# Performance work log

Hardware: AMD Instinct MI355X
Metric: run time of the kernel (lower is better)

The kernel has to match this reference:

```python
import jax, jax.numpy as jnp
import numpy as np

B, H, S, D = 2, 8, 4096, 64

def setup_inputs() -> dict:
    key = jax.random.key(0)
    kq, kk, kv = jax.random.split(key, 3)
    queries = jax.random.normal(kq, (B, H, S, D), dtype=jnp.float32)
    keys = jax.random.normal(kk, (B, H, S, D), dtype=jnp.float32)
    values = jax.random.normal(kv, (B, H, S, D), dtype=jnp.float32)
    adj = jnp.zeros((1,), dtype=jnp.int32)  # unused by the module, kept for signature fidelity
    return {"queries": queries, "keys": keys, "values": values, "adj": adj}

def reference(queries, keys, values, adj):
    # scores: [B,H,S,S]; note the original divides by a hard-coded 16, not sqrt(d)
    scores = jnp.einsum('bhqd,bhkd->bhqk', queries, keys) / 16.0
    attn = jax.nn.softmax(scores, axis=-1)
    # dropout p=0.0 -> identity in eval/deterministic mode
    h = jnp.einsum('bhqk,bhkd->bhqd', attn, values)  # [B,H,S,D]
    # original uses .view (a reshape, NOT a transpose) to (S, B, H, D)
    return jnp.reshape(h, (S, B, H, D))
```

## Files before the change

kernel.cpp:

```cpp
#include <hip/hip_runtime.h>
#include <hip/hip_bf16.h>
#include <math.h>

#define S_LEN 4096
#define D_DIM 64
#define NBH   16
#define HKT   32
#define QPRE  0.09016844f

typedef __attribute__((ext_vector_type(8))) short bf16x8;
typedef __attribute__((ext_vector_type(4))) float f32x4;
typedef __attribute__((ext_vector_type(4))) __fp16 f16x4;
typedef __attribute__((ext_vector_type(2))) __fp16 f16x2;

__device__ __forceinline__ unsigned int pkbf(float lo, float hi) {
  unsigned int ua = __float_as_uint(lo) + 0x8000u;
  unsigned int ub = __float_as_uint(hi) + 0x8000u;
  return __builtin_amdgcn_perm(ub, ua, 0x07060302u);
}
__device__ __forceinline__ unsigned int pkhf(float lo, float hi) {
  f16x2 h = __builtin_amdgcn_cvt_pkrtz(lo, hi);
  return *(unsigned int*)&h;
}
__device__ __forceinline__ void dma16(const unsigned short* g, unsigned short* l) {
  __builtin_amdgcn_global_load_lds(
      (const __attribute__((address_space(1))) unsigned int*)g,
      (__attribute__((address_space(3))) unsigned int*)l, 16, 0, 0);
}

__global__ __launch_bounds__(256) void prep(const float* __restrict__ K,
                                            const float* __restrict__ V,
                                            unsigned short* __restrict__ Kbf,
                                            unsigned short* __restrict__ Vt) {
  const int tid = threadIdx.x;
  __shared__ unsigned short tile[64][72];
  if (blockIdx.x < 256) {
    const int bh = blockIdx.x >> 4, ch = blockIdx.x & 15;
    const size_t base = ((size_t)bh * S_LEN + ch * 256) * D_DIM;
#pragma unroll
    for (int p = 0; p < 8; ++p) {
      int i = tid + p * 256;
      int row = i >> 3, c = (i & 7) * 8;
      float4 a = *(const float4*)&K[base + row * D_DIM + c];
      float4 b = *(const float4*)&K[base + row * D_DIM + c + 4];
      uint4 w;
      w.x = pkbf(a.x, a.y); w.y = pkbf(a.z, a.w);
      w.z = pkbf(b.x, b.y); w.w = pkbf(b.z, b.w);
      *(uint4*)&Kbf[base + row * D_DIM + c] = w;
    }
    return;
  }
  const int blk = blockIdx.x - 256;
  const int bh = blk >> 6, kt = blk & 63;
  const float* src = V + ((size_t)bh * S_LEN + kt * 64) * D_DIM;
#pragma unroll
  for (int p = 0; p < 4; ++p) {
    int i = tid + p * 256;
    int row = i >> 4, c = (i & 15) * 4;
    float4 f = *(const float4*)&src[row * D_DIM + c];
    int cs = c ^ (((row >> 4) & 3) << 4);
    unsigned long long w = (unsigned long long)pkhf(f.x, f.y) |
                           ((unsigned long long)pkhf(f.z, f.w) << 32);
    *(unsigned long long*)&tile[row][cs] = w;
  }
  __syncthreads();
  const int kc = tid & 7;
#pragma unroll
  for (int p = 0; p < 2; ++p) {
    int d = p * 32 + (tid >> 3);
    int col = d ^ (((kc >> 1) & 3) << 4);
    union { unsigned short u[8]; uint4 v; } t;
#pragma unroll
    for (int i = 0; i < 8; ++i) t.u[i] = tile[kc * 8 + i][col];
    *(uint4*)&Vt[((size_t)bh * D_DIM + d) * S_LEN + kt * 64 + kc * 8] = t.v;
  }
}

__global__ __launch_bounds__(256, 4) void fattn(const float* __restrict__ Q,
                                                const unsigned short* __restrict__ Kbf,
                                                const unsigned short* __restrict__ Vt,
                                                unsigned short* __restrict__ Oh,
                                                float* __restrict__ Lw) {
  const int bh   = blockIdx.x & 15;
  const int qb   = (blockIdx.x >> 4) & 31;
  const int half = blockIdx.x >> 9;
  const int tid  = threadIdx.x;
  const int wave = tid >> 6;
  const int lane = tid & 63;
  const int quad = lane >> 4;
  const int l15  = lane & 15;
  const int rho  = l15 & 7;
  const int T0   = half * HKT;

  __shared__ unsigned short Ksh[2][64][64];
  __shared__ unsigned short Vsh[2][64][64];

  bf16x8 qf[2][2];
#pragma unroll
  for (int qt = 0; qt < 2; ++qt) {
    const int qg = qb * 128 + wave * 32 + qt * 16 + l15;
    const float* qp = Q + ((size_t)bh * S_LEN + qg) * D_DIM + quad * 8;
#pragma unroll
    for (int h = 0; h < 2; ++h) {
      float4 a = *(const float4*)&qp[h * 32];
      float4 b = *(const float4*)&qp[h * 32 + 4];
      union { unsigned int u[4]; bf16x8 v; } f;
      f.u[0] = pkbf(a.x * QPRE, a.y * QPRE);
      f.u[1] = pkbf(a.z * QPRE, a.w * QPRE);
      f.u[2] = pkbf(b.x * QPRE, b.y * QPRE);
      f.u[3] = pkbf(b.z * QPRE, b.w * QPRE);
      qf[qt][h] = f.v;
    }
  }

  f32x4 ot[2][4];
#pragma unroll
  for (int qt = 0; qt < 2; ++qt)
#pragma unroll
    for (int dt = 0; dt < 4; ++dt) ot[qt][dt] = (f32x4){0.f, 0.f, 0.f, 0.f};
  float Lp[2] = {0.f, 0.f};

  const unsigned short* Kb = Kbf + (size_t)bh * S_LEN * D_DIM;
  const unsigned short* Vb = Vt + (size_t)bh * D_DIM * S_LEN;

  const int r_lo = wave * 8 + (lane >> 3);
  const int csrc = ((lane & 7) ^ (lane >> 3)) * 8;

  const int ck0 = (quad ^ rho) * 8;
  const int ck1 = ((quad + 4) ^ rho) * 8;
  const int vrow  = l15 * 128 + (quad & 1) * 8;
  const int rho16 = rho << 4;
  const int vq2   = (quad >> 1) << 4;

#define DMAK(T, B) do { const int t_ = (T); \
  dma16(&Kb[(size_t)(t_ * 64 + r_lo) * 64 + csrc],      &Ksh[B][wave * 8][0]); \
  dma16(&Kb[(size_t)(t_ * 64 + r_lo + 32) * 64 + csrc], &Ksh[B][wave * 8 + 32][0]); } while (0)
#define DMAV(T, B) do { const int t_ = (T); \
  dma16(&Vb[(size_t)r_lo * S_LEN + t_ * 64 + csrc],        &Vsh[B][wave * 8][0]); \
  dma16(&Vb[(size_t)(r_lo + 32) * S_LEN + t_ * 64 + csrc], &Vsh[B][wave * 8 + 32][0]); } while (0)

#define SCORES(KB, PD) do { \
  _Pragma("unroll") \
  for (int mt = 0; mt < 4; ++mt) { \
    const int row_ = mt * 16 + l15; \
    bf16x8 kf0 = *(const bf16x8*)&Ksh[KB][row_][ck0]; \
    bf16x8 kf1 = *(const bf16x8*)&Ksh[KB][row_][ck1]; \
    _Pragma("unroll") \
    for (int qt = 0; qt < 2; ++qt) { \
      f32x4 acc = (f32x4){0.f, 0.f, 0.f, 0.f}; \
      acc = __builtin_amdgcn_mfma_f32_16x16x32_bf16(kf0, qf[qt][0], acc, 0, 0, 0); \
      acc = __builtin_amdgcn_mfma_f32_16x16x32_bf16(kf1, qf[qt][1], acc, 0, 0, 0); \
      float p0 = __builtin_amdgcn_exp2f(acc[0]); \
      float p1 = __builtin_amdgcn_exp2f(acc[1]); \
      float p2 = __builtin_amdgcn_exp2f(acc[2]); \
      float p3 = __builtin_amdgcn_exp2f(acc[3]); \
      Lp[qt] += (p0 + p1) + (p2 + p3); \
      PD[mt][qt][0] = pkhf(p0, p1); \
      PD[mt][qt][1] = pkhf(p2, p3); \
    } \
  } } while (0)

#define PVSTEP(VB, PU) do { \
  const char* vbase = (const char*)&Vsh[VB][0][0]; \
  _Pragma("unroll") \
  for (int mt = 0; mt < 4; ++mt) { \
    const int vb_ = vrow + (((mt << 5) + vq2) ^ rho16); \
    union { unsigned int u[2]; f16x4 v; } pb0, pb1; \
    pb0.u[0] = PU[mt][0][0]; pb0.u[1] = PU[mt][0][1]; \
    pb1.u[0] = PU[mt][1][0]; pb1.u[1] = PU[mt][1][1]; \
    _Pragma("unroll") \
    for (int dt = 0; dt < 4; ++dt) { \
      f16x4 va = *(const f16x4*)(vbase + vb_ + dt * 2048); \
      ot[0][dt] = __builtin_amdgcn_mfma_f32_16x16x16f16(va, pb0.v, ot[0][dt], 0, 0, 0); \
      ot[1][dt] = __builtin_amdgcn_mfma_f32_16x16x16f16(va, pb1.v, ot[1][dt], 0, 0, 0); \
    } \
  } } while (0)

#define ITER(I, KBL, KBU, VBL, VBU, PU, PD) do { \
  __syncthreads(); \
  if ((I) < HKT - 2) DMAK(T0 + (I) + 2, KBL); \
  DMAV(T0 + (I) + 1, VBL); \
  SCORES(KBU, PD); \
  PVSTEP(VBU, PU); } while (0)

  unsigned int pA[4][2][2], pB[4][2][2];

  DMAK(T0, 0); DMAV(T0, 0);
  __syncthreads();
  SCORES(0, pA);
  DMAK(T0 + 1, 1);

  for (int b = 0; b < HKT - 2; b += 2) {
    ITER(b + 0, 0, 1, 1, 0, pA, pB);
    ITER(b + 1, 1, 0, 0, 1, pB, pA);
  }
  ITER(HKT - 2, 0, 1, 1, 0, pA, pB);
  __syncthreads();
  PVSTEP(1, pB);

#pragma unroll
  for (int qt = 0; qt < 2; ++qt) {
    float Lt = Lp[qt];
    Lt += __shfl_xor(Lt, 16);
    Lt += __shfl_xor(Lt, 32);
    const size_t grow = (size_t)bh * S_LEN + qb * 128 + wave * 32 + qt * 16 + l15;
    if (quad == 0) Lw[grow * 2 + half] = Lt;
#pragma unroll
    for (int dt = 0; dt < 4; ++dt) {
      uint2 w;
      w.x = pkhf(ot[qt][dt][0], ot[qt][dt][1]);
      w.y = pkhf(ot[qt][dt][2], ot[qt][dt][3]);
      *(uint2*)&Oh[grow * 128 + half * 64 + dt * 16 + quad * 4] = w;
    }
  }
#undef DMAK
#undef DMAV
#undef SCORES
#undef PVSTEP
#undef ITER
}

__global__ __launch_bounds__(256) void reduce(unsigned short* Oh, const float* __restrict__ Lw) {
  const int tid = threadIdx.x;
  const size_t r = (size_t)blockIdx.x * 32 + (tid >> 3);
  const int d0 = (tid & 7) * 8;
  union { uint4 v; __fp16 h[8]; } a, b;
  a.v = *(const uint4*)&Oh[r * 128 + d0];
  b.v = *(const uint4*)&Oh[r * 128 + 64 + d0];
  const float linv = 1.0f / (Lw[r * 2] + Lw[r * 2 + 1]);
  float o[8];
#pragma unroll
  for (int j = 0; j < 8; ++j) o[j] = ((float)a.h[j] + (float)b.h[j]) * linv;
  __syncthreads();
  float* Of = (float*)Oh;
  float4 w0 = {o[0], o[1], o[2], o[3]};
  float4 w1 = {o[4], o[5], o[6], o[7]};
  *(float4*)&Of[r * 64 + d0]     = w0;
  *(float4*)&Of[r * 64 + d0 + 4] = w1;
}

extern "C" void kernel_launch(void* const* d_in, const int* in_sizes, int n_in,
                              void* d_out, int out_size, void* d_ws, size_t ws_size,
                              hipStream_t stream) {
  const float* Q = (const float*)d_in[0];
  const float* K = (const float*)d_in[1];
  const float* V = (const float*)d_in[2];
  unsigned short* Kbf = (unsigned short*)d_ws;
  unsigned short* Vt  = Kbf + (size_t)NBH * S_LEN * D_DIM;
  float* Lw = (float*)(Vt + (size_t)NBH * S_LEN * D_DIM);
  unsigned short* Oh = (unsigned short*)d_out;

  prep<<<1280, 256, 0, stream>>>(K, V, Kbf, Vt);
  fattn<<<NBH * 32 * 2, 256, 0, stream>>>(Q, Kbf, Vt, Oh, Lw);
  reduce<<<(NBH * S_LEN) / 32, 256, 0, stream>>>(Oh, Lw);
}
```

Before: 184.3 us.

## Switch attention MFMAs to 32x32x16 tiles with permlane32 swap for P layout

```diff
diff --git a/kernel.cpp b/kernel.cpp
--- a/kernel.cpp
+++ b/kernel.cpp
@@ -10,8 +10,10 @@
 
 typedef __attribute__((ext_vector_type(8))) short bf16x8;
 typedef __attribute__((ext_vector_type(4))) float f32x4;
-typedef __attribute__((ext_vector_type(4))) __fp16 f16x4;
+typedef __attribute__((ext_vector_type(16))) float f32x16;
+typedef __attribute__((ext_vector_type(8))) __fp16 f16x8;
 typedef __attribute__((ext_vector_type(2))) __fp16 f16x2;
+typedef __attribute__((ext_vector_type(2))) unsigned int u32x2;
 
 __device__ __forceinline__ unsigned int pkbf(float lo, float hi) {
   unsigned int ua = __float_as_uint(lo) + 0x8000u;
@@ -87,50 +89,38 @@
   const int tid  = threadIdx.x;
   const int wave = tid >> 6;
   const int lane = tid & 63;
-  const int quad = lane >> 4;
-  const int l15  = lane & 15;
-  const int rho  = l15 & 7;
+  const int l31  = lane & 31;
+  const int hi   = lane >> 5;
   const int T0   = half * HKT;
 
   __shared__ unsigned short Ksh[2][64][64];
   __shared__ unsigned short Vsh[2][64][64];
 
-  bf16x8 qf[2][2];
-#pragma unroll
-  for (int qt = 0; qt < 2; ++qt) {
-    const int qg = qb * 128 + wave * 32 + qt * 16 + l15;
-    const float* qp = Q + ((size_t)bh * S_LEN + qg) * D_DIM + quad * 8;
-#pragma unroll
-    for (int h = 0; h < 2; ++h) {
-      float4 a = *(const float4*)&qp[h * 32];
-      float4 b = *(const float4*)&qp[h * 32 + 4];
+  bf16x8 qf2[4];
+  {
+    const int qg = qb * 128 + wave * 32 + l31;
+    const float* qp = Q + ((size_t)bh * S_LEN + qg) * D_DIM + hi * 8;
+#pragma unroll
+    for (int dm = 0; dm < 4; ++dm) {
+      float4 a = *(const float4*)&qp[dm * 16];
+      float4 b = *(const float4*)&qp[dm * 16 + 4];
       union { unsigned int u[4]; bf16x8 v; } f;
       f.u[0] = pkbf(a.x * QPRE, a.y * QPRE);
       f.u[1] = pkbf(a.z * QPRE, a.w * QPRE);
       f.u[2] = pkbf(b.x * QPRE, b.y * QPRE);
       f.u[3] = pkbf(b.z * QPRE, b.w * QPRE);
-      qf[qt][h] = f.v;
+      qf2[dm] = f.v;
     }
   }
 
-  f32x4 ot[2][4];
-#pragma unroll
-  for (int qt = 0; qt < 2; ++qt)
-#pragma unroll
-    for (int dt = 0; dt < 4; ++dt) ot[qt][dt] = (f32x4){0.f, 0.f, 0.f, 0.f};
-  float Lp[2] = {0.f, 0.f};
+  f32x16 ov[2] = {{}, {}};
+  float Lt = 0.f;
 
   const unsigned short* Kb = Kbf + (size_t)bh * S_LEN * D_DIM;
   const unsigned short* Vb = Vt + (size_t)bh * D_DIM * S_LEN;
 
   const int r_lo = wave * 8 + (lane >> 3);
   const int csrc = ((lane & 7) ^ (lane >> 3)) * 8;
-
-  const int ck0 = (quad ^ rho) * 8;
-  const int ck1 = ((quad + 4) ^ rho) * 8;
-  const int vrow  = l15 * 128 + (quad & 1) * 8;
-  const int rho16 = rho << 4;
-  const int vq2   = (quad >> 1) << 4;
 
 #define DMAK(T, B) do { const int t_ = (T); \
   dma16(&Kb[(size_t)(t_ * 64 + r_lo) * 64 + csrc],      &Ksh[B][wave * 8][0]); \
@@ -140,39 +130,47 @@
   dma16(&Vb[(size_t)(r_lo + 32) * S_LEN + t_ * 64 + csrc], &Vsh[B][wave * 8 + 32][0]); } while (0)
 
 #define SCORES(KB, PD) do { \
+  const char* kbase_ = (const char*)&Ksh[KB][0][0]; \
   _Pragma("unroll") \
-  for (int mt = 0; mt < 4; ++mt) { \
-    const int row_ = mt * 16 + l15; \
-    bf16x8 kf0 = *(const bf16x8*)&Ksh[KB][row_][ck0]; \
-    bf16x8 kf1 = *(const bf16x8*)&Ksh[KB][row_][ck1]; \
+  for (int kt2 = 0; kt2 < 2; ++kt2) { \
+    const int krow_ = kt2 * 32 + l31; \
+    f32x16 acc2 = {}; \
     _Pragma("unroll") \
-    for (int qt = 0; qt < 2; ++qt) { \
-      f32x4 acc = (f32x4){0.f, 0.f, 0.f, 0.f}; \
-      acc = __builtin_amdgcn_mfma_f32_16x16x32_bf16(kf0, qf[qt][0], acc, 0, 0, 0); \
-      acc = __builtin_amdgcn_mfma_f32_16x16x32_bf16(kf1, qf[qt][1], acc, 0, 0, 0); \
-      float p0 = __builtin_amdgcn_exp2f(acc[0]); \
-      float p1 = __builtin_amdgcn_exp2f(acc[1]); \
-      float p2 = __builtin_amdgcn_exp2f(acc[2]); \
-      float p3 = __builtin_amdgcn_exp2f(acc[3]); \
-      Lp[qt] += (p0 + p1) + (p2 + p3); \
-      PD[mt][qt][0] = pkhf(p0, p1); \
-      PD[mt][qt][1] = pkhf(p2, p3); \
+    for (int dm = 0; dm < 4; ++dm) { \
+      bf16x8 kf = *(const bf16x8*)(kbase_ + krow_ * 128 + (((dm * 2 + hi) ^ (krow_ & 7)) * 16)); \
+      acc2 = __builtin_amdgcn_mfma_f32_32x32x16_bf16(kf, qf2[dm], acc2, 0, 0, 0); \
     } \
+    float pp[16]; \
+    _Pragma("unroll") \
+    for (int j = 0; j < 16; ++j) pp[j] = __builtin_amdgcn_exp2f(acc2[j]); \
+    Lt += (((pp[0] + pp[1]) + (pp[2] + pp[3])) + ((pp[4] + pp[5]) + (pp[6] + pp[7]))) \
+        + (((pp[8] + pp[9]) + (pp[10] + pp[11])) + ((pp[12] + pp[13]) + (pp[14] + pp[15]))); \
+    unsigned int w00 = pkhf(pp[0], pp[1]),   w01 = pkhf(pp[2], pp[3]); \
+    unsigned int w10 = pkhf(pp[4], pp[5]),   w11 = pkhf(pp[6], pp[7]); \
+    unsigned int w20 = pkhf(pp[8], pp[9]),   w21 = pkhf(pp[10], pp[11]); \
+    unsigned int w30 = pkhf(pp[12], pp[13]), w31 = pkhf(pp[14], pp[15]); \
+    u32x2 s0 = __builtin_amdgcn_permlane32_swap(w00, w10, false, false); \
+    u32x2 s1 = __builtin_amdgcn_permlane32_swap(w01, w11, false, false); \
+    u32x2 s2 = __builtin_amdgcn_permlane32_swap(w20, w30, false, false); \
+    u32x2 s3 = __builtin_amdgcn_permlane32_swap(w21, w31, false, false); \
+    PD[kt2 * 2 + 0][0] = s0.x; PD[kt2 * 2 + 0][1] = s1.x; \
+    PD[kt2 * 2 + 0][2] = s0.y; PD[kt2 * 2 + 0][3] = s1.y; \
+    PD[kt2 * 2 + 1][0] = s2.x; PD[kt2 * 2 + 1][1] = s3.x; \
+    PD[kt2 * 2 + 1][2] = s2.y; PD[kt2 * 2 + 1][3] = s3.y; \
   } } while (0)
 
 #define PVSTEP(VB, PU) do { \
-  const char* vbase = (const char*)&Vsh[VB][0][0]; \
+  const char* vbase_ = (const char*)&Vsh[VB][0][0]; \
   _Pragma("unroll") \
-  for (int mt = 0; mt < 4; ++mt) { \
-    const int vb_ = vrow + (((mt << 5) + vq2) ^ rho16); \
-    union { unsigned int u[2]; f16x4 v; } pb0, pb1; \
-    pb0.u[0] = PU[mt][0][0]; pb0.u[1] = PU[mt][0][1]; \
-    pb1.u[0] = PU[mt][1][0]; pb1.u[1] = PU[mt][1][1]; \
+  for (int dt2 = 0; dt2 < 2; ++dt2) { \
+    const int drow_ = dt2 * 32 + l31; \
     _Pragma("unroll") \
-    for (int dt = 0; dt < 4; ++dt) { \
-      f16x4 va = *(const f16x4*)(vbase + vb_ + dt * 2048); \
-      ot[0][dt] = __builtin_amdgcn_mfma_f32_16x16x16f16(va, pb0.v, ot[0][dt], 0, 0, 0); \
-      ot[1][dt] = __builtin_amdgcn_mfma_f32_16x16x16f16(va, pb1.v, ot[1][dt], 0, 0, 0); \
+    for (int s4 = 0; s4 < 4; ++s4) { \
+      f16x8 va = *(const f16x8*)(vbase_ + drow_ * 128 + (((s4 * 2 + hi) ^ (drow_ & 7)) * 16)); \
+      union { unsigned int u[4]; f16x8 v; } pb; \
+      pb.u[0] = PU[s4][0]; pb.u[1] = PU[s4][1]; \
+      pb.u[2] = PU[s4][2]; pb.u[3] = PU[s4][3]; \
+      ov[dt2] = __builtin_amdgcn_mfma_f32_32x32x16_f16(va, pb.v, ov[dt2], 0, 0, 0); \
     } \
   } } while (0)
 
@@ -183,7 +181,7 @@
   SCORES(KBU, PD); \
   PVSTEP(VBU, PU); } while (0)
 
-  unsigned int pA[4][2][2], pB[4][2][2];
+  unsigned int pA[4][4], pB[4][4];
 
   DMAK(T0, 0); DMAV(T0, 0);
   __syncthreads();
@@ -198,21 +196,18 @@
   __syncthreads();
   PVSTEP(1, pB);
 
-#pragma unroll
-  for (int qt = 0; qt < 2; ++qt) {
-    float Lt = Lp[qt];
-    Lt += __shfl_xor(Lt, 16);
-    Lt += __shfl_xor(Lt, 32);
-    const size_t grow = (size_t)bh * S_LEN + qb * 128 + wave * 32 + qt * 16 + l15;
-    if (quad == 0) Lw[grow * 2 + half] = Lt;
-#pragma unroll
-    for (int dt = 0; dt < 4; ++dt) {
+  Lt += __shfl_xor(Lt, 32);
+  const size_t grow = (size_t)bh * S_LEN + qb * 128 + wave * 32 + l31;
+  if (lane < 32) Lw[grow * 2 + half] = Lt;
+#pragma unroll
+  for (int dt2 = 0; dt2 < 2; ++dt2)
+#pragma unroll
+    for (int m = 0; m < 4; ++m) {
       uint2 w;
-      w.x = pkhf(ot[qt][dt][0], ot[qt][dt][1]);
-      w.y = pkhf(ot[qt][dt][2], ot[qt][dt][3]);
-      *(uint2*)&Oh[grow * 128 + half * 64 + dt * 16 + quad * 4] = w;
+      w.x = pkhf(ov[dt2][4 * m + 0], ov[dt2][4 * m + 1]);
+      w.y = pkhf(ov[dt2][4 * m + 2], ov[dt2][4 * m + 3]);
+      *(uint2*)&Oh[grow * 128 + half * 64 + dt2 * 32 + m * 8 + hi * 4] = w;
     }
-  }
 #undef DMAK
 #undef DMAV
 #undef SCORES
```

Measured after the change: 215.5 us. +17.0%, slower.
